# Kernel tuning notes

Hardware: AMD Instinct MI355X
Metric: run time of the kernel (lower is better)

## Reference

```python
import jax, jax.numpy as jnp
import numpy as np

V, E, H, L = 80, 8, 256, 2
B, S = 2048, 256


def setup_inputs() -> dict:
    key = jax.random.key(0)
    ks = jax.random.split(key, 8)
    x = jax.random.randint(ks[0], (B, S), 0, V, dtype=jnp.int32)
    emb = jax.random.normal(ks[1], (V, E), jnp.float32) * 0.1

    def cell_params(k, din):
        k1, k2 = jax.random.split(k)
        W_ih = jax.random.normal(k1, (4 * H, din), jnp.float32) * (1.0 / np.sqrt(din))
        W_hh = jax.random.normal(k2, (4 * H, H), jnp.float32) * (1.0 / np.sqrt(H))
        # biases zero except forget gate (second quarter) set to 1, as in _initialize_weights
        b_ih = jnp.zeros((4 * H,), jnp.float32).at[H:2 * H].set(1.0)
        b_hh = jnp.zeros((4 * H,), jnp.float32).at[H:2 * H].set(1.0)
        return W_ih, W_hh, b_ih, b_hh

    W_ih0, W_hh0, b_ih0, b_hh0 = cell_params(ks[2], E)
    W_ih1, W_hh1, b_ih1, b_hh1 = cell_params(ks[3], H)
    fc_w = jax.random.normal(ks[4], (V, H), jnp.float32) * (1.0 / np.sqrt(H))
    fc_b = jnp.zeros((V,), jnp.float32)
    return dict(x=x, emb=emb,
                W_ih0=W_ih0, W_hh0=W_hh0, b_ih0=b_ih0, b_hh0=b_hh0,
                W_ih1=W_ih1, W_hh1=W_hh1, b_ih1=b_ih1, b_hh1=b_hh1,
                fc_w=fc_w, fc_b=fc_b)


def _lstm_cell(x_t, h, c, W_ih, W_hh, b_ih, b_hh):
    # PyTorch LSTMCell gate order: i, f, g, o
    gates = x_t @ W_ih.T + b_ih + h @ W_hh.T + b_hh  # [B, 4H]
    i_g, f_g, g_g, o_g = jnp.split(gates, 4, axis=-1)
    c_new = jax.nn.sigmoid(f_g) * c + jax.nn.sigmoid(i_g) * jnp.tanh(g_g)
    h_new = jax.nn.sigmoid(o_g) * jnp.tanh(c_new)
    return h_new, c_new


def reference(x, emb, W_ih0, W_hh0, b_ih0, b_hh0, W_ih1, W_hh1, b_ih1, b_hh1, fc_w, fc_b):
    batch = x.shape[0]
    layers = ((W_ih0, W_hh0, b_ih0, b_hh0), (W_ih1, W_hh1, b_ih1, b_hh1))
    e = emb[x]                       # [B, S, E]
    e_t = jnp.swapaxes(e, 0, 1)      # [S, B, E] time-major for scan

    h0 = tuple(jnp.zeros((batch, H), e.dtype) for _ in range(L))
    c0 = tuple(jnp.zeros((batch, H), e.dtype) for _ in range(L))

    def step(carry, x_t):
        hs, cs = carry
        inp = x_t
        new_h, new_c = [], []
        for i, (Wi, Wh, bi, bh) in enumerate(layers):
            h_i, c_i = _lstm_cell(inp, hs[i], cs[i], Wi, Wh, bi, bh)
            new_h.append(h_i)
            new_c.append(c_i)
            inp = h_i
        return (tuple(new_h), tuple(new_c)), None

    (h_fin, c_fin), _ = jax.lax.scan(step, (h0, c0), e_t)
    # dropout is identity in eval mode; fc on last layer's final hidden state
    logits = h_fin[-1] @ fc_w.T + fc_b    # [B, V]
    return logits, (jnp.stack(h_fin), jnp.stack(c_fin))
```

## Files before the change

kernel.cpp:

```cpp
#include <hip/hip_runtime.h>
#include <math.h>

#define VCAB 80
#define EDIM 8
#define HDIM 256
#define BAT 2048
#define SEQ 256
#define BT 8
#define NWG (BAT/BT)
#define NTHR 1024
#define KG 4

#define W0T_KP 272
#define W1T_K 512
#define W0T_OFF 0
#define W1T_OFF (W0T_KP*1024)
#define BIAS0_OFF (W1T_OFF + W1T_K*1024)
#define BIAS1_OFF (BIAS0_OFF + 1024)
#define WS_FLOATS (BIAS1_OFF + 1024)

__global__ void prep_kernel(const float* __restrict__ Wih0, const float* __restrict__ Whh0,
                            const float* __restrict__ bih0, const float* __restrict__ bhh0,
                            const float* __restrict__ Wih1, const float* __restrict__ Whh1,
                            const float* __restrict__ bih1, const float* __restrict__ bhh1,
                            float* __restrict__ ws) {
  int idx = blockIdx.x * 256 + threadIdx.x;
  if (idx < W0T_KP * 1024) {
    int k = idx >> 10, n2 = idx & 1023;
    int unit = n2 >> 2, g = n2 & 3, r = g * HDIM + unit;
    float v = (k < EDIM) ? Wih0[r * EDIM + k]
            : (k < EDIM + HDIM) ? Whh0[r * HDIM + (k - EDIM)]
            : 0.f;
    ws[W0T_OFF + idx] = v;
  } else if (idx < W0T_KP * 1024 + W1T_K * 1024) {
    int i2 = idx - W0T_KP * 1024;
    int k = i2 >> 10, n2 = i2 & 1023;
    int unit = n2 >> 2, g = n2 & 3, r = g * HDIM + unit;
    float v = (k < HDIM) ? Wih1[r * HDIM + k] : Whh1[r * HDIM + (k - HDIM)];
    ws[W1T_OFF + i2] = v;
  } else if (idx < W0T_KP * 1024 + W1T_K * 1024 + 1024) {
    int n2 = idx - (W0T_KP * 1024 + W1T_K * 1024);
    int unit = n2 >> 2, g = n2 & 3, r = g * HDIM + unit;
    ws[BIAS0_OFF + n2] = bih0[r] + bhh0[r];
  } else if (idx < W0T_KP * 1024 + W1T_K * 1024 + 2048) {
    int n2 = idx - (W0T_KP * 1024 + W1T_K * 1024 + 1024);
    int unit = n2 >> 2, g = n2 & 3, r = g * HDIM + unit;
    ws[BIAS1_OFF + n2] = bih1[r] + bhh1[r];
  }
}

__device__ __forceinline__ float sigm(float x) {
  return 1.0f / (1.0f + __expf(-x));
}
__device__ __forceinline__ float tanh_f(float x) {
  float ax = fabsf(x);
  float e = __expf(-2.0f * ax);
  float t = 1.0f - 2.0f * e / (1.0f + e);
  return copysignf(t, x);
}

#define FMA4(A, HS, W) \
  A.x += (HS) * (W).x; A.y += (HS) * (W).y; A.z += (HS) * (W).z; A.w += (HS) * (W).w;

__global__ __launch_bounds__(NTHR, 4) void lstm_kernel(
    const int* __restrict__ x, const float* __restrict__ emb,
    const float* __restrict__ ws,
    const float* __restrict__ fcw, const float* __restrict__ fcb,
    float* __restrict__ out) {
  __shared__ float inp0[BT][W0T_KP];
  __shared__ float inp1[BT][W1T_K];
  __shared__ float4 red[KG - 1][BT][HDIM];

  const int tid = threadIdx.x;
  const int utid = tid & 255;
  const int kgrp = tid >> 8;
  const int bg = blockIdx.x * BT;
  const float4* __restrict__ W0 = (const float4*)(ws + W0T_OFF);
  const float4* __restrict__ W1 = (const float4*)(ws + W1T_OFF);

  float c0[BT], c1[BT];
#pragma unroll
  for (int b = 0; b < BT; b++) { c0[b] = 0.f; c1[b] = 0.f; }
  if (kgrp == 0) {
#pragma unroll
    for (int b = 0; b < BT; b++) {
      inp0[b][EDIM + utid] = 0.f;
      inp1[b][utid] = 0.f;
      inp1[b][HDIM + utid] = 0.f;
    }
  }
  if (tid < BT * EDIM) inp0[tid >> 3][264 + (tid & 7)] = 0.f;
  const float4 bias0 = ((const float4*)(ws + BIAS0_OFF))[utid];
  const float4 bias1 = ((const float4*)(ws + BIAS1_OFF))[utid];
  __syncthreads();

  for (int t = 0; t < SEQ; t++) {
    if (tid < BT * EDIM) {
      int b = tid >> 3, d = tid & 7;
      int xv = x[(bg + b) * SEQ + t];
      inp0[b][d] = emb[xv * EDIM + d];
    }
    __syncthreads();

    float4 acc[BT];
#pragma unroll
    for (int b = 0; b < BT; b++) acc[b] = make_float4(0.f, 0.f, 0.f, 0.f);
    {
      const int kbase = kgrp * (W0T_KP / KG);
#pragma unroll 2
      for (int i = 0; i < W0T_KP / KG / 4; i++) {
        const int k = kbase + 4 * i;
        float4 wa = W0[(k + 0) * 256 + utid];
        float4 wb = W0[(k + 1) * 256 + utid];
        float4 wc = W0[(k + 2) * 256 + utid];
        float4 wd = W0[(k + 3) * 256 + utid];
#pragma unroll
        for (int b = 0; b < BT; b++) {
          float4 hv = *(const float4*)&inp0[b][k];
          FMA4(acc[b], hv.x, wa); FMA4(acc[b], hv.y, wb);
          FMA4(acc[b], hv.z, wc); FMA4(acc[b], hv.w, wd);
        }
      }
    }
    if (kgrp > 0) {
#pragma unroll
      for (int b = 0; b < BT; b++) red[kgrp - 1][b][utid] = acc[b];
    }
    __syncthreads();
    if (kgrp == 0) {
#pragma unroll
      for (int b = 0; b < BT; b++) {
        float4 p0 = red[0][b][utid], p1 = red[1][b][utid], p2 = red[2][b][utid];
        float gx = acc[b].x + p0.x + p1.x + p2.x + bias0.x;
        float gy = acc[b].y + p0.y + p1.y + p2.y + bias0.y;
        float gz = acc[b].z + p0.z + p1.z + p2.z + bias0.z;
        float gw = acc[b].w + p0.w + p1.w + p2.w + bias0.w;
        float ig = sigm(gx), fg = sigm(gy), gg = tanh_f(gz), og = sigm(gw);
        c0[b] = fg * c0[b] + ig * gg;
        float h = og * tanh_f(c0[b]);
        inp0[b][EDIM + utid] = h;
        inp1[b][utid] = h;
      }
    }
    __syncthreads();

#pragma unroll
    for (int b = 0; b < BT; b++) acc[b] = make_float4(0.f, 0.f, 0.f, 0.f);
    {
      const int kbase = kgrp * (W1T_K / KG);
#pragma unroll 2
      for (int i = 0; i < W1T_K / KG / 4; i++) {
        const int k = kbase + 4 * i;
        float4 wa = W1[(k + 0) * 256 + utid];
        float4 wb = W1[(k + 1) * 256 + utid];
        float4 wc = W1[(k + 2) * 256 + utid];
        float4 wd = W1[(k + 3) * 256 + utid];
#pragma unroll
        for (int b = 0; b < BT; b++) {
          float4 hv = *(const float4*)&inp1[b][k];
          FMA4(acc[b], hv.x, wa); FMA4(acc[b], hv.y, wb);
          FMA4(acc[b], hv.z, wc); FMA4(acc[b], hv.w, wd);
        }
      }
    }
    if (kgrp > 0) {
#pragma unroll
      for (int b = 0; b < BT; b++) red[kgrp - 1][b][utid] = acc[b];
    }
    __syncthreads();
    if (kgrp == 0) {
#pragma unroll
      for (int b = 0; b < BT; b++) {
        float4 p0 = red[0][b][utid], p1 = red[1][b][utid], p2 = red[2][b][utid];
        float gx = acc[b].x + p0.x + p1.x + p2.x + bias1.x;
        float gy = acc[b].y + p0.y + p1.y + p2.y + bias1.y;
        float gz = acc[b].z + p0.z + p1.z + p2.z + bias1.z;
        float gw = acc[b].w + p0.w + p1.w + p2.w + bias1.w;
        float ig = sigm(gx), fg = sigm(gy), gg = tanh_f(gz), og = sigm(gw);
        c1[b] = fg * c1[b] + ig * gg;
        inp1[b][HDIM + utid] = og * tanh_f(c1[b]);
      }
    }
    __syncthreads();
  }

  for (int o = tid; o < BT * VCAB; o += NTHR) {
    int b = o / VCAB, v = o - b * VCAB;
    float a = fcb[v];
    const float4* wrow = (const float4*)(fcw + v * HDIM);
    const float4* hrow = (const float4*)&inp1[b][HDIM];
#pragma unroll 4
    for (int k = 0; k < HDIM / 4; k++) {
      float4 w = wrow[k];
      float4 h = hrow[k];
      a += h.x * w.x + h.y * w.y + h.z * w.z + h.w * w.w;
    }
    out[(bg + b) * VCAB + v] = a;
  }

  if (kgrp == 0) {
    float* outh = out + BAT * VCAB;
    float* outc = outh + 2 * BAT * HDIM;
#pragma unroll
    for (int b = 0; b < BT; b++) {
      outh[0 * BAT * HDIM + (bg + b) * HDIM + utid] = inp0[b][EDIM + utid];
      outh[1 * BAT * HDIM + (bg + b) * HDIM + utid] = inp1[b][HDIM + utid];
      outc[0 * BAT * HDIM + (bg + b) * HDIM + utid] = c0[b];
      outc[1 * BAT * HDIM + (bg + b) * HDIM + utid] = c1[b];
    }
  }
}

extern "C" void kernel_launch(void* const* d_in, const int* in_sizes, int n_in,
                              void* d_out, int out_size, void* d_ws, size_t ws_size,
                              hipStream_t stream) {
  const int*   x    = (const int*)d_in[0];
  const float* emb  = (const float*)d_in[1];
  const float* Wih0 = (const float*)d_in[2];
  const float* Whh0 = (const float*)d_in[3];
  const float* bih0 = (const float*)d_in[4];
  const float* bhh0 = (const float*)d_in[5];
  const float* Wih1 = (const float*)d_in[6];
  const float* Whh1 = (const float*)d_in[7];
  const float* bih1 = (const float*)d_in[8];
  const float* bhh1 = (const float*)d_in[9];
  const float* fcw  = (const float*)d_in[10];
  const float* fcb  = (const float*)d_in[11];
  float* out = (float*)d_out;
  float* ws  = (float*)d_ws;

  prep_kernel<<<(WS_FLOATS + 255) / 256, 256, 0, stream>>>(
      Wih0, Whh0, bih0, bhh0, Wih1, Whh1, bih1, bhh1, ws);
  lstm_kernel<<<NWG, NTHR, 0, stream>>>(x, emb, ws, fcw, fcb, out);
}
```

Baseline: 13.70 ms.

## Distribute gate reduction and activations across all k-groups, prefetch next embedding

Previously k-group 0 alone reduced partial sums and ran the LSTM activations for all 8 batch rows while the other three groups sat idle. Now each k-group owns two batch rows, writes the partials other groups need, and reduces and activates its own rows, so the epilogue work is split four ways. The embedding load for step t+1 is also folded into the layer-0 epilogue, which removes one barrier per timestep. Shared-memory traffic for the partials stays about the same, and the change adds some index arithmetic.

Measured after the change: 17.96 ms. 1.31x slower.

```diff
diff --git a/kernel.cpp b/kernel.cpp
--- a/kernel.cpp
+++ b/kernel.cpp
@@ -75,33 +75,29 @@
   const int utid = tid & 255;
   const int kgrp = tid >> 8;
   const int bg = blockIdx.x * BT;
+  const int r0 = 2 * kgrp;
   const float4* __restrict__ W0 = (const float4*)(ws + W0T_OFF);
   const float4* __restrict__ W1 = (const float4*)(ws + W1T_OFF);
 
-  float c0[BT], c1[BT];
-#pragma unroll
-  for (int b = 0; b < BT; b++) { c0[b] = 0.f; c1[b] = 0.f; }
-  if (kgrp == 0) {
-#pragma unroll
-    for (int b = 0; b < BT; b++) {
-      inp0[b][EDIM + utid] = 0.f;
-      inp1[b][utid] = 0.f;
-      inp1[b][HDIM + utid] = 0.f;
-    }
-  }
-  if (tid < BT * EDIM) inp0[tid >> 3][264 + (tid & 7)] = 0.f;
+  float c0[2], c1[2];
+  c0[0] = c0[1] = c1[0] = c1[1] = 0.f;
+#pragma unroll
+  for (int j = 0; j < 2; j++) {
+    inp0[r0 + j][EDIM + utid] = 0.f;
+    inp1[r0 + j][utid] = 0.f;
+    inp1[r0 + j][HDIM + utid] = 0.f;
+  }
+  if (tid < BT * EDIM) {
+    int b = tid >> 3, d = tid & 7;
+    inp0[b][264 + d] = 0.f;
+    int xv = x[(bg + b) * SEQ + 0];
+    inp0[b][d] = emb[xv * EDIM + d];
+  }
   const float4 bias0 = ((const float4*)(ws + BIAS0_OFF))[utid];
   const float4 bias1 = ((const float4*)(ws + BIAS1_OFF))[utid];
   __syncthreads();
 
   for (int t = 0; t < SEQ; t++) {
-    if (tid < BT * EDIM) {
-      int b = tid >> 3, d = tid & 7;
-      int xv = x[(bg + b) * SEQ + t];
-      inp0[b][d] = emb[xv * EDIM + d];
-    }
-    __syncthreads();
-
     float4 acc[BT];
 #pragma unroll
     for (int b = 0; b < BT; b++) acc[b] = make_float4(0.f, 0.f, 0.f, 0.f);
@@ -122,25 +118,31 @@
         }
       }
     }
-    if (kgrp > 0) {
-#pragma unroll
-      for (int b = 0; b < BT; b++) red[kgrp - 1][b][utid] = acc[b];
-    }
-    __syncthreads();
-    if (kgrp == 0) {
-#pragma unroll
-      for (int b = 0; b < BT; b++) {
-        float4 p0 = red[0][b][utid], p1 = red[1][b][utid], p2 = red[2][b][utid];
-        float gx = acc[b].x + p0.x + p1.x + p2.x + bias0.x;
-        float gy = acc[b].y + p0.y + p1.y + p2.y + bias0.y;
-        float gz = acc[b].z + p0.z + p1.z + p2.z + bias0.z;
-        float gw = acc[b].w + p0.w + p1.w + p2.w + bias0.w;
-        float ig = sigm(gx), fg = sigm(gy), gg = tanh_f(gz), og = sigm(gw);
-        c0[b] = fg * c0[b] + ig * gg;
-        float h = og * tanh_f(c0[b]);
-        inp0[b][EDIM + utid] = h;
-        inp1[b][utid] = h;
-      }
+#pragma unroll
+    for (int r = 0; r < BT; r++) {
+      int o = r >> 1;
+      if (o != kgrp) red[kgrp - (kgrp > o ? 1 : 0)][r][utid] = acc[r];
+    }
+    __syncthreads();
+
+#pragma unroll
+    for (int j = 0; j < 2; j++) {
+      int r = r0 + j;
+      float4 p0 = red[0][r][utid], p1 = red[1][r][utid], p2 = red[2][r][utid];
+      float gx = acc[r].x + p0.x + p1.x + p2.x + bias0.x;
+      float gy = acc[r].y + p0.y + p1.y + p2.y + bias0.y;
+      float gz = acc[r].z + p0.z + p1.z + p2.z + bias0.z;
+      float gw = acc[r].w + p0.w + p1.w + p2.w + bias0.w;
+      float ig = sigm(gx), fg = sigm(gy), gg = tanh_f(gz), og = sigm(gw);
+      c0[j] = fg * c0[j] + ig * gg;
+      float h = og * tanh_f(c0[j]);
+      inp0[r][EDIM + utid] = h;
+      inp1[r][utid] = h;
+    }
+    if (t + 1 < SEQ && tid < BT * EDIM) {
+      int b = tid >> 3, d = tid & 7;
+      int xv = x[(bg + b) * SEQ + t + 1];
+      inp0[b][d] = emb[xv * EDIM + d];
     }
     __syncthreads();
 
@@ -163,23 +165,24 @@
         }
       }
     }
-    if (kgrp > 0) {
-#pragma unroll
-      for (int b = 0; b < BT; b++) red[kgrp - 1][b][utid] = acc[b];
-    }
-    __syncthreads();
-    if (kgrp == 0) {
-#pragma unroll
-      for (int b = 0; b < BT; b++) {
-        float4 p0 = red[0][b][utid], p1 = red[1][b][utid], p2 = red[2][b][utid];
-        float gx = acc[b].x + p0.x + p1.x + p2.x + bias1.x;
-        float gy = acc[b].y + p0.y + p1.y + p2.y + bias1.y;
-        float gz = acc[b].z + p0.z + p1.z + p2.z + bias1.z;
-        float gw = acc[b].w + p0.w + p1.w + p2.w + bias1.w;
-        float ig = sigm(gx), fg = sigm(gy), gg = tanh_f(gz), og = sigm(gw);
-        c1[b] = fg * c1[b] + ig * gg;
-        inp1[b][HDIM + utid] = og * tanh_f(c1[b]);
-      }
+#pragma unroll
+    for (int r = 0; r < BT; r++) {
+      int o = r >> 1;
+      if (o != kgrp) red[kgrp - (kgrp > o ? 1 : 0)][r][utid] = acc[r];
+    }
+    __syncthreads();
+
+#pragma unroll
+    for (int j = 0; j < 2; j++) {
+      int r = r0 + j;
+      float4 p0 = red[0][r][utid], p1 = red[1][r][utid], p2 = red[2][r][utid];
+      float gx = acc[r].x + p0.x + p1.x + p2.x + bias1.x;
+      float gy = acc[r].y + p0.y + p1.y + p2.y + bias1.y;
+      float gz = acc[r].z + p0.z + p1.z + p2.z + bias1.z;
+      float gw = acc[r].w + p0.w + p1.w + p2.w + bias1.w;
+      float ig = sigm(gx), fg = sigm(gy), gg = tanh_f(gz), og = sigm(gw);
+      c1[j] = fg * c1[j] + ig * gg;
+      inp1[r][HDIM + utid] = og * tanh_f(c1[j]);
     }
     __syncthreads();
   }
@@ -198,15 +201,16 @@
     out[(bg + b) * VCAB + v] = a;
   }
 
-  if (kgrp == 0) {
+  {
     float* outh = out + BAT * VCAB;
     float* outc = outh + 2 * BAT * HDIM;
 #pragma unroll
-    for (int b = 0; b < BT; b++) {
+    for (int j = 0; j < 2; j++) {
+      int b = r0 + j;
       outh[0 * BAT * HDIM + (bg + b) * HDIM + utid] = inp0[b][EDIM + utid];
       outh[1 * BAT * HDIM + (bg + b) * HDIM + utid] = inp1[b][HDIM + utid];
-      outc[0 * BAT * HDIM + (bg + b) * HDIM + utid] = c0[b];
-      outc[1 * BAT * HDIM + (bg + b) * HDIM + utid] = c1[b];
+      outc[0 * BAT * HDIM + (bg + b) * HDIM + utid] = c0[j];
+      outc[1 * BAT * HDIM + (bg + b) * HDIM + utid] = c1[j];
     }
   }
 }
```
